# Kernel tuning notes

Measured on AMD Instinct MI355X. Metric: run time of the kernel, lower is better.

The kernel has to match this reference:

```python
import jax, jax.numpy as jnp
import numpy as np

B, S, H, DK, DV, DE = 2, 256, 8, 64, 64, 512
DT = H * DV
EPS = 1e-5

def _clin(xr, xi, W, b):
    # complex linear: x @ W + b with (re, im) parts; W: (2, d_in, d_out), b: (2, d_out)
    yr = xr @ W[0] - xi @ W[1] + b[0]
    yi = xr @ W[1] + xi @ W[0] + b[1]
    return yr, yi

def _emul(ar, ai, br, bi):
    # complex elementwise (Hadamard) multiply
    return ar * br - ai * bi, ar * bi + ai * br

def _forward(Z_q, Z_k, Z_v, t_measure_all, Wq, bq, Wk, bk, Wv, bv, Wp, bp,
             lambda_imag_v, lambda_real_v, lambda_omega_sqrt_v,
             lambda_gamma_sqrt_v, noise_floor, tau, eta_param):
    Bn = Z_q.shape[0]
    t = t_measure_all[0, :-1]
    t = t / (t[-1] - t[0])

    def heads(z, W, b, d):
        yr, yi = _clin(z[:, 0], z[:, 1], W, b)
        f = lambda a: a.reshape(Bn, S, H, d).swapaxes(-1, -2)  # (B,S,d,H)
        return f(yr), f(yi)

    Qr, Qi = heads(Z_q, Wq, bq, DK)
    Kr, Ki = heads(Z_k, Wk, bk, DK)
    Vr, Vi = heads(Z_v, Wv, bv, DV)

    # complex eigenvalues in conjugate pairs: (DV, H)
    lam_im = jnp.concatenate([lambda_imag_v, -lambda_imag_v], axis=1).T
    lam_re = jnp.broadcast_to(lambda_real_v[None, :], (DV, H))

    # forward/backward exponential kernels exp(+/- lambda t): (S, DV, H)
    phase = t[:, None, None] * lam_im[None]
    mag = jnp.exp(t[:, None, None] * lam_re[None])
    ef_r = mag * jnp.cos(phase); ef_i = mag * jnp.sin(phase)
    eb_r = jnp.cos(phase) / mag; eb_i = -jnp.sin(phase) / mag
    me_r, me_i = ef_r[0], ef_i[0]  # mat_exp

    # scalar covariance kernel per (i, j, head): process noise + measurement noise
    omega = lambda_omega_sqrt_v ** 2
    gamma = lambda_gamma_sqrt_v ** 2 + EPS
    dt = jnp.maximum(t[:, None] - t[None, :], 0.0)  # causal lags only
    den = 2.0 * lambda_real_v  # (H,)
    safe = jnp.where(jnp.abs(den) > 1e-6, den, 1.0)
    x = dt[:, :, None] * den
    g = jnp.where(jnp.abs(den) > 1e-6, jnp.expm1(x) / safe, dt[:, :, None])
    V_avg = omega * g + gamma * jnp.exp(x)  # (S,S,H)

    # factorized kernels: U_* = exp(-lambda t_j) * X_j ; propagator factor |exp(lambda t_i)|^2
    Uq_r, Uq_i = _emul(eb_r[None], eb_i[None], Qr, Qi)
    Uk_r, Uk_i = _emul(eb_r[None], eb_i[None], Kr, Ki)
    Uv_r, Uv_i = _emul(eb_r[None], eb_i[None], Vr, Vi)
    Vk2 = ef_r ** 2 + ef_i ** 2  # (S,DV,H)

    # precision-weighted residual norm |exp(lambda(t_i-t_j)) k_j - q_i|^2
    Uq2 = Uq_r ** 2 + Uq_i ** 2
    Uk2 = Uk_r ** 2 + Uk_i ** 2
    self_q = jnp.einsum('idh,bidh->bih', Vk2, Uq2)
    term_k = jnp.einsum('idh,bjdh->bijh', Vk2, Uk2)
    cross = (jnp.einsum('bidh,bjdh->bijh', Vk2[None] * Uq_r, Uk_r)
             + jnp.einsum('bidh,bjdh->bijh', Vk2[None] * Uq_i, Uk_i))
    R = term_k + self_q[:, :, None, :] - 2.0 * cross  # (B,S,S,H)

    base = (noise_floor ** 2 + EPS) * V_avg[None] + R
    scores = -(tau ** 2) * jnp.log(base)
    mask = jnp.tril(jnp.ones((S, S), bool))
    scores = jnp.where(mask[None, :, :, None], scores, -jnp.inf)
    attn = jax.nn.softmax(scores, axis=2)  # (B,S,S,H)

    # complex matmul with real-valued attention (imag part of Q_ij is zero)
    er = jnp.einsum('bijh,bjdh->bidh', attn, Uv_r)
    ei = jnp.einsum('bijh,bjdh->bidh', attn, Uv_i)
    est_r, est_i = _emul(ef_r[None], ef_i[None], er, ei)

    eta = jax.nn.sigmoid(eta_param)[0, 0]  # (1,DV,H)
    el_r = (1.0 - eta) * Vr + jax.nn.sigmoid(eta) * est_r
    el_i = (1.0 - eta) * Vi + jax.nn.sigmoid(eta) * est_i

    pr, pi = _emul(me_r[None, None], me_i[None, None], el_r, el_i)
    merge = lambda a: a.swapaxes(-1, -2).reshape(Bn, S, DT)
    o_r, o_i = _clin(merge(pr), merge(pi), Wp, bp)
    out = jnp.stack([o_r, o_i], axis=1)  # (B,2,S,DE)

    # all-pairs propagated estimates Z_ij = exp(lambda t_i) * U_v,j
    zr, zi = _emul(ef_r[None, :, None], ef_i[None, :, None],
                   Uv_r[:, None], Uv_i[:, None])  # (B,S,S,DV,H)
    zm = lambda a: a.swapaxes(-1, -2).reshape(Bn, S, S, DT)
    Z_ij = jnp.stack([zm(zr), zm(zi)], axis=1)  # (B,2,S,S,DT)

    est_latent = jnp.stack([el_r, el_i], axis=1)  # (B,2,S,DV,H)
    Q_ij = jnp.stack([attn, jnp.zeros_like(attn)], axis=1)
    epoch_lambdas = jnp.stack([lam_re, lam_im], 0).swapaxes(-1, -2).reshape(2, H * DV)[..., None]
    return est_latent, out, Q_ij, Z_ij, epoch_lambdas

def setup_inputs():
    key = jax.random.key(0)
    k = jax.random.split(key, 16)
    sc_in = 1.0 / np.sqrt(DE)
    sc_out = 1.0 / np.sqrt(DT)
    return {
        'Z_q': jax.random.normal(k[0], (B, 2, S, DE), jnp.float32),
        'Z_k': jax.random.normal(k[1], (B, 2, S, DE), jnp.float32),
        'Z_v': jax.random.normal(k[2], (B, 2, S, DE), jnp.float32),
        't_measure_all': jnp.arange(S + 1, dtype=jnp.float32)[None, :],
        'Wq': jax.random.normal(k[3], (2, DE, DT), jnp.float32) * sc_in,
        'bq': jax.random.normal(k[4], (2, DT), jnp.float32) * 0.01,
        'Wk': jax.random.normal(k[5], (2, DE, DT), jnp.float32) * sc_in,
        'bk': jax.random.normal(k[6], (2, DT), jnp.float32) * 0.01,
        'Wv': jax.random.normal(k[7], (2, DE, DT), jnp.float32) * sc_in,
        'bv': jax.random.normal(k[8], (2, DT), jnp.float32) * 0.01,
        'Wp': jax.random.normal(k[9], (2, DT, DE), jnp.float32) * sc_out,
        'bp': jax.random.normal(k[10], (2, DE), jnp.float32) * 0.01,
        'lambda_imag_v': jax.random.normal(k[11], (H, DV // 2), jnp.float32),
        'lambda_real_v': jax.random.normal(k[12], (H,), jnp.float32) * 0.5,
        'lambda_omega_sqrt_v': jax.random.normal(k[13], (H,), jnp.float32),
        'lambda_gamma_sqrt_v': jax.random.normal(k[14], (H,), jnp.float32),
        'noise_floor': jnp.ones((H,), jnp.float32),
        'tau': jnp.ones((H,), jnp.float32),
        'eta_param': jnp.zeros((1, 1, 1, DV, H), jnp.float32),
    }

def reference(Z_q, Z_k, Z_v, t_measure_all, Wq, bq, Wk, bk, Wv, bv, Wp, bp,
              lambda_imag_v, lambda_real_v, lambda_omega_sqrt_v,
              lambda_gamma_sqrt_v, noise_floor, tau, eta_param):
    return _forward(Z_q, Z_k, Z_v, t_measure_all, Wq, bq, Wk, bk, Wv, bv, Wp, bp,
                    lambda_imag_v, lambda_real_v, lambda_omega_sqrt_v,
                    lambda_gamma_sqrt_v, noise_floor, tau, eta_param)
```

## Files before the change

### kernel.cpp

```cpp
#include <hip/hip_runtime.h>
#include <hip/hip_bf16.h>
#include <math.h>

constexpr int kB  = 2;
constexpr int kS  = 256;
constexpr int kH  = 8;
constexpr float kEPS = 1e-5f;

constexpr int OFF_EST = 0;
constexpr int OFF_OUT = 524288;
constexpr int OFF_QIJ = 1048576;
constexpr int OFF_ZIJ = 3145728;
constexpr int OFF_EPO = 137363456;

constexpr int WS_EFR = 0;
constexpr int WS_EFI = 131072;
constexpr int WS_EBR = 262144;
constexpr int WS_EBI = 393216;
constexpr int WS_UQR = 524288;
constexpr int WS_UQI = 786432;
constexpr int WS_UKR = 1048576;
constexpr int WS_UKI = 1310720;
constexpr int WS_UVR = 1572864;
constexpr int WS_UVI = 1835008;
constexpr int WS_VR  = 2097152;
constexpr int WS_VI  = 2359296;
constexpr int WS_BF  = 3145728;

constexpr int A2Q = 0;
constexpr int A2K = 524288;
constexpr int A2V = 1048576;
constexpr int B2R0 = 1572864;

typedef __attribute__((ext_vector_type(8))) short bf16x8;
typedef __attribute__((ext_vector_type(4))) float f32x4;
typedef __attribute__((ext_vector_type(8))) unsigned short u16x8;
typedef __attribute__((ext_vector_type(4))) unsigned short u16x4;

__device__ __forceinline__ float sigm(float x) { return 1.f / (1.f + expf(-x)); }
__device__ __forceinline__ unsigned short f2b(float f) {
    __hip_bfloat16 h = __float2bfloat16(f);
    return *reinterpret_cast<unsigned short*>(&h);
}

__global__ __launch_bounds__(256) void k_precompute(
    const float* __restrict__ tall, const float* __restrict__ Lim,
    const float* __restrict__ Lre,
    float* __restrict__ efr, float* __restrict__ efi,
    float* __restrict__ ebr, float* __restrict__ ebi,
    float* __restrict__ epo)
{
    int idx = blockIdx.x * 256 + threadIdx.x;
    int s = idx >> 9;
    int c = idx & 511;
    int h = c >> 6;
    int d = c & 63;
    float li = (d < 32) ? Lim[h * 32 + d] : -Lim[h * 32 + d - 32];
    float lr = Lre[h];
    float t  = tall[s] / (tall[kS - 1] - tall[0]);
    float ph  = t * li;
    float mag = expf(t * lr);
    float cp  = cosf(ph);
    float sp  = sinf(ph);
    efr[idx] = mag * cp;
    efi[idx] = mag * sp;
    ebr[idx] = cp / mag;
    ebi[idx] = -sp / mag;
    if (s == 0) {
        epo[c]       = lr;
        epo[512 + c] = li;
    }
}

__global__ __launch_bounds__(256) void k_convA(
    const float* __restrict__ zq, const float* __restrict__ zk,
    const float* __restrict__ zv, __hip_bfloat16* __restrict__ bfbase)
{
    int idx = blockIdx.x * 256 + threadIdx.x;
    int tz  = idx >> 16;
    int rem = idx & 65535;
    int m   = rem >> 7;
    int k0  = (rem & 127) * 8;
    const float* src = (tz == 0) ? zq : (tz == 1) ? zk : zv;
    int b = m >> 8, s = m & 255;
    int c = (k0 >= 512) ? 1 : 0;
    int e = k0 - c * 512;
    const float* p = src + ((b * 2 + c) * 256 + s) * 512 + e;
    float4 v0 = *(const float4*)p;
    float4 v1 = *(const float4*)(p + 4);
    u16x8 o;
    o[0] = f2b(v0.x); o[1] = f2b(v0.y); o[2] = f2b(v0.z); o[3] = f2b(v0.w);
    o[4] = f2b(v1.x); o[5] = f2b(v1.y); o[6] = f2b(v1.z); o[7] = f2b(v1.w);
    __hip_bfloat16* dst = bfbase + ((tz == 0) ? A2Q : (tz == 1) ? A2K : A2V)
                          + m * 1024 + k0;
    *(u16x8*)dst = o;
}

__global__ __launch_bounds__(256) void k_convW(
    const float* __restrict__ wq, const float* __restrict__ wk,
    const float* __restrict__ wv, const float* __restrict__ wp,
    __hip_bfloat16* __restrict__ bfbase)
{
    __shared__ float s0[64][65];
    __shared__ float s1[64][65];
    const int z = blockIdx.z;
    const float* W  = (z == 0) ? wq : (z == 1) ? wk : (z == 2) ? wv : wp;
    const float* W0 = W;
    const float* W1 = W + 262144;
    const int k0 = blockIdx.x * 64;
    const int n0 = blockIdx.y * 64;
    const int kp = k0 & 511;
    const bool hf = (k0 >= 512);
    const int t = threadIdx.x;
    const int r = t >> 2;
    const int q = t & 3;
#pragma unroll
    for (int c = 0; c < 4; ++c) {
        int col = q * 16 + c * 4;
        *(float4*)&s0[r][col] = *(const float4*)&W0[(kp + r) * 512 + n0 + col];
        *(float4*)&s1[r][col] = *(const float4*)&W1[(kp + r) * 512 + n0 + col];
    }
    __syncthreads();
    u16x8 r0, r1, i0, i1;
#pragma unroll
    for (int u = 0; u < 8; ++u) {
        int kl = q * 16 + u;
        float w0 = s0[kl][r], w1 = s1[kl][r];
        r0[u] = f2b(hf ? -w1 : w0);
        i0[u] = f2b(hf ?  w0 : w1);
    }
#pragma unroll
    for (int u = 0; u < 8; ++u) {
        int kl = q * 16 + 8 + u;
        float w0 = s0[kl][r], w1 = s1[kl][r];
        r1[u] = f2b(hf ? -w1 : w0);
        i1[u] = f2b(hf ?  w0 : w1);
    }
    __hip_bfloat16* pr = bfbase + B2R0 + z * 1048576
                         + (size_t)(n0 + r) * 1024 + k0 + q * 16;
    __hip_bfloat16* pi = pr + 524288;
    *(u16x8*)pr       = r0;
    *(u16x8*)(pr + 8) = r1;
    *(u16x8*)pi       = i0;
    *(u16x8*)(pi + 8) = i1;
}

template<bool IS_P>
__global__ __launch_bounds__(256) void k_cmfma(
    const __hip_bfloat16* __restrict__ bfbase,
    const __hip_bfloat16* __restrict__ a2p,
    const float* __restrict__ bq, const float* __restrict__ bk,
    const float* __restrict__ bv, const float* __restrict__ bp,
    const float* __restrict__ ebr, const float* __restrict__ ebi,
    float* __restrict__ uqr, float* __restrict__ uqi,
    float* __restrict__ ukr, float* __restrict__ uki,
    float* __restrict__ uvr, float* __restrict__ uvi,
    float* __restrict__ vr,  float* __restrict__ vi,
    float* __restrict__ outp)
{
    __shared__ __align__(16) char sm[24576];
    char* sA  = sm;
    char* sBr = sm + 8192;
    char* sBi = sm + 16384;

    const int mode = IS_P ? 3 : (int)blockIdx.z;
    const __hip_bfloat16* A2 = IS_P ? a2p
        : bfbase + ((mode == 0) ? A2Q : (mode == 1) ? A2K : A2V);
    const __hip_bfloat16* Br = bfbase + B2R0 + mode * 1048576;
    const __hip_bfloat16* Bi = Br + 524288;
    const float* bias = IS_P ? bp : ((mode == 0) ? bq : (mode == 1) ? bk : bv);

    const int tid = threadIdx.x;
    const int m0 = blockIdx.y * 64;
    const int n0 = blockIdx.x * 64;
    const int lane = tid & 63;
    const int wv2 = tid >> 6;
    const int wr = wv2 >> 1, wc = wv2 & 1;
    const int lx = lane & 15, lhi = lane >> 4;

    const int srow  = tid >> 2;
    const int sslot = (tid & 3) * 32;

    const char* gA  = (const char*)(A2 + (size_t)(m0 + srow) * 1024);
    const char* gBr = (const char*)(Br + (size_t)(n0 + srow) * 1024);
    const char* gBi = (const char*)(Bi + (size_t)(n0 + srow) * 1024);
    const int swz = (srow & 7) << 4;
    char* dA  = sA  + srow * 128;
    char* dBr = sBr + srow * 128;
    char* dBi = sBi + srow * 128;

    f32x4 accR[2][2] = {};
    f32x4 accI[2][2] = {};

    int rowA[2], rowB[2];
    rowA[0] = wr * 32 + lx;  rowA[1] = rowA[0] + 16;
    rowB[0] = wc * 32 + lx;  rowB[1] = rowB[0] + 16;

    for (int kt = 0; kt < 16; ++kt) {
        const int kb = kt * 128;
        {
            float4 a0 = *(const float4*)(gA  + kb + sslot);
            float4 a1 = *(const float4*)(gA  + kb + sslot + 16);
            float4 b0 = *(const float4*)(gBr + kb + sslot);
            float4 b1 = *(const float4*)(gBr + kb + sslot + 16);
            float4 c0 = *(const float4*)(gBi + kb + sslot);
            float4 c1 = *(const float4*)(gBi + kb + sslot + 16);
            *(float4*)(dA  + ( sslot       ^ swz)) = a0;
            *(float4*)(dA  + ((sslot + 16) ^ swz)) = a1;
            *(float4*)(dBr + ( sslot       ^ swz)) = b0;
            *(float4*)(dBr + ((sslot + 16) ^ swz)) = b1;
            *(float4*)(dBi + ( sslot       ^ swz)) = c0;
            *(float4*)(dBi + ((sslot + 16) ^ swz)) = c1;
        }
        __syncthreads();
#pragma unroll
        for (int kk = 0; kk < 2; ++kk) {
            const int kbyte = kk * 64 + lhi * 16;
            bf16x8 af[2], brf[2], bif[2];
#pragma unroll
            for (int x = 0; x < 2; ++x) {
                int ra = rowA[x];
                af[x]  = *(const bf16x8*)(sA  + ra * 128 + (kbyte ^ ((ra & 7) << 4)));
                int rb = rowB[x];
                brf[x] = *(const bf16x8*)(sBr + rb * 128 + (kbyte ^ ((rb & 7) << 4)));
                bif[x] = *(const bf16x8*)(sBi + rb * 128 + (kbyte ^ ((rb & 7) << 4)));
            }
#pragma unroll
            for (int a = 0; a < 2; ++a)
#pragma unroll
                for (int bb = 0; bb < 2; ++bb) {
                    accR[a][bb] = __builtin_amdgcn_mfma_f32_16x16x32_bf16(
                        af[a], brf[bb], accR[a][bb], 0, 0, 0);
                    accI[a][bb] = __builtin_amdgcn_mfma_f32_16x16x32_bf16(
                        af[a], bif[bb], accI[a][bb], 0, 0, 0);
                }
        }
        __syncthreads();
    }

#pragma unroll
    for (int a = 0; a < 2; ++a) {
#pragma unroll
        for (int bb = 0; bb < 2; ++bb) {
#pragma unroll
            for (int j = 0; j < 4; ++j) {
                int m = m0 + wr * 32 + a * 16 + lhi * 4 + j;
                int n = n0 + wc * 32 + bb * 16 + lx;
                float yr = accR[a][bb][j] + bias[n];
                float yi = accI[a][bb][j] + bias[512 + n];
                int b = m >> 8, s = m & 255;
                if (IS_P) {
                    int rowo = m * 512 + b * 131072;
                    outp[rowo + n] = yr;
                    outp[rowo + 131072 + n] = yi;
                } else {
                    int h = n >> 6, d = n & 63;
                    float er_ = ebr[s * 512 + n], ei_ = ebi[s * 512 + n];
                    float ur = er_ * yr - ei_ * yi;
                    float ui = er_ * yi + ei_ * yr;
                    if (mode == 0) {
                        int idx = ((b * 8 + h) * 256 + s) * 64 + d;
                        uqr[idx] = ur; uqi[idx] = ui;
                    } else if (mode == 1) {
                        int idx = ((b * 8 + h) * 64 + d) * 256 + s;
                        ukr[idx] = ur; uki[idx] = ui;
                    } else {
                        int idx = ((b * 8 + h) * 256 + s) * 64 + d;
                        uvr[idx] = ur; uvi[idx] = ui;
                        int vidx = (b * 256 + s) * 512 + d * 8 + h;
                        vr[vidx] = yr; vi[vidx] = yi;
                    }
                }
            }
        }
    }
}

__global__ __launch_bounds__(256) void k_scores(
    const float* __restrict__ uqr, const float* __restrict__ uqi,
    const float* __restrict__ ukr, const float* __restrict__ uki,
    const float* __restrict__ tall,
    const float* __restrict__ Lre, const float* __restrict__ Lom,
    const float* __restrict__ Lga, const float* __restrict__ NF,
    const float* __restrict__ TAU,
    float* __restrict__ qij)
{
    __shared__ __align__(16) float sQr[32][68];
    __shared__ __align__(16) float sQi[32][68];
    __shared__ __align__(16) float sKr[64][32];
    __shared__ __align__(16) float sKi[64][32];

    int p = blockIdx.x;
    int it = 0;
    while (p > it) { p -= (it + 1); ++it; }
    const int jt = p;

    const int h = blockIdx.y, b = blockIdx.z;
    const int i0 = it * 32;
    const int j0 = jt * 32;
    const int tid = threadIdx.x;
    const int ti = tid >> 3;
    const int tj = tid & 7;

    {
        const float* src_r = uqr + ((b * 8 + h) * 256 + i0 + ti) * 64;
        const float* src_i = uqi + ((b * 8 + h) * 256 + i0 + ti) * 64;
        *(float4*)&sQr[ti][tj * 4]      = *(const float4*)&src_r[tj * 4];
        *(float4*)&sQr[ti][32 + tj * 4] = *(const float4*)&src_r[32 + tj * 4];
        *(float4*)&sQi[ti][tj * 4]      = *(const float4*)&src_i[tj * 4];
        *(float4*)&sQi[ti][32 + tj * 4] = *(const float4*)&src_i[32 + tj * 4];
    }
    {
        const int kr2 = tid >> 2;
        const int kq2 = tid & 3;
        const float* ksrc_r = ukr + ((b * 8 + h) * 64 + kr2) * 256 + j0;
        const float* ksrc_i = uki + ((b * 8 + h) * 64 + kr2) * 256 + j0;
        *(float4*)&sKr[kr2][kq2 * 4]      = *(const float4*)&ksrc_r[kq2 * 4];
        *(float4*)&sKr[kr2][16 + kq2 * 4] = *(const float4*)&ksrc_r[16 + kq2 * 4];
        *(float4*)&sKi[kr2][kq2 * 4]      = *(const float4*)&ksrc_i[kq2 * 4];
        *(float4*)&sKi[kr2][16 + kq2 * 4] = *(const float4*)&ksrc_i[16 + kq2 * 4];
    }

    const float lre  = Lre[h];
    const float om   = Lom[h] * Lom[h];
    const float ga   = Lga[h] * Lga[h] + kEPS;
    const float nf2  = NF[h] * NF[h] + kEPS;
    const float tau2 = TAU[h] * TAU[h];
    const float den  = 2.f * lre;
    const float invT = 1.f / (tall[kS - 1] - tall[0]);
    const int   i    = i0 + ti;
    const float t_i  = tall[i] * invT;
    const float m2i  = expf(2.f * t_i * lre);
    const bool  denok = fabsf(den) > 1e-6f;

    __syncthreads();

    float acc[4] = {0.f, 0.f, 0.f, 0.f};
#pragma unroll 16
    for (int d = 0; d < 64; d++) {
        float qr = sQr[ti][d];
        float qi = sQi[ti][d];
        float4 kr = *(float4*)&sKr[d][tj * 4];
        float4 ki = *(float4*)&sKi[d][tj * 4];
#define DSTEP(c, KRC, KIC)                                    \
        { float dr = qr - KRC; float di = qi - KIC;           \
          acc[c] = fmaf(dr, dr, acc[c]);                      \
          acc[c] = fmaf(di, di, acc[c]); }
        DSTEP(0, kr.x, ki.x)
        DSTEP(1, kr.y, ki.y)
        DSTEP(2, kr.z, ki.z)
        DSTEP(3, kr.w, ki.w)
#undef DSTEP
    }

#pragma unroll
    for (int c = 0; c < 4; c++) {
        int j = j0 + tj * 4 + c;
        if (j <= i) {
            float t_j = tall[j] * invT;
            float dtt = fmaxf(t_i - t_j, 0.f);
            float x = dtt * den;
            float g = denok ? (expm1f(x) / den) : dtt;
            float Vv = om * g + ga * expf(x);
            float base = nf2 * Vv + m2i * acc[c];
            qij[((b * 512 + i) * 256 + j) * 8 + h] = -tau2 * logf(base);
        }
    }
}

__global__ __launch_bounds__(256) void k_zij_smpv(
    const float* __restrict__ efr, const float* __restrict__ efi,
    const float* __restrict__ uvr, const float* __restrict__ uvi,
    float* __restrict__ zout,
    float* __restrict__ qij,
    const float* __restrict__ vr,  const float* __restrict__ vi,
    const float* __restrict__ ETA,
    float* __restrict__ out_est, __hip_bfloat16* __restrict__ a2p)
{
    __shared__ float sP[32][257];
    __shared__ __align__(16) float sVr[32][64];
    __shared__ __align__(16) float sVi[32][64];

    const int bid = blockIdx.x;
    const int tid = threadIdx.x;

    if (bid >= 128) {
        const int z  = bid - 128;
        const int j0 = (z & 63) * 4;
        const int i  = (z >> 6) & 255;
        const int b  = z >> 14;
#pragma unroll
        for (int half = 0; half < 2; half++) {
            int dt = half * 256 + tid;
            float fr = efr[i * 512 + dt];
            float fi = efi[i * 512 + dt];
            int h = dt >> 6, d = dt & 63;
            const float* ur = uvr + ((b * 8 + h) * 256) * 64 + d;
            const float* ui = uvi + ((b * 8 + h) * 256) * 64 + d;
#pragma unroll
            for (int jj = 0; jj < 4; jj++) {
                int j = j0 + jj;
                float vr_ = ur[j * 64];
                float vi_ = ui[j * 64];
                float zr = fr * vr_ - fi * vi_;
                float zi = fr * vi_ + fi * vr_;
                int idx0 = (b * 2) * 33554432 + i * 131072 + j * 512 + dt;
                __builtin_nontemporal_store(zr, &zout[idx0]);
                __builtin_nontemporal_store(zi, &zout[idx0 + 33554432]);
            }
        }
        return;
    }

    const int it = bid & 7;
    const int h  = (bid >> 3) & 7;
    const int b  = bid >> 6;
    const int i0 = it * 32;
    const int ti = tid >> 3;
    const int tj = tid & 7;
    const int i  = i0 + ti;

    float* srow = qij + ((b * 512 + i) * 256) * 8 + h;
    float mx = -1e30f;
    for (int j = tj; j <= i; j += 8) {
        float v = srow[j * 8];
        sP[ti][j] = v;
        mx = fmaxf(mx, v);
    }
#pragma unroll
    for (int m = 1; m < 8; m <<= 1) mx = fmaxf(mx, __shfl_xor(mx, m));
    float sum = 0.f;
    for (int j = tj; j <= i; j += 8) {
        float e = expf(sP[ti][j] - mx);
        sP[ti][j] = e;
        sum += e;
    }
#pragma unroll
    for (int m = 1; m < 8; m <<= 1) sum += __shfl_xor(sum, m);
    const float inv = 1.f / sum;

    float* qi_out = qij + ((b * 512 + 256 + i) * 256) * 8 + h;
    const int jfill = i0 + 32;
    for (int j = tj; j < 256; j += 8) {
        float p = 0.f;
        if (j <= i) p = sP[ti][j] * inv;
        if (j < jfill) sP[ti][j] = p;
        srow[j * 8]   = p;
        qi_out[j * 8] = 0.f;
    }
    __syncthreads();

    const int dl = tid & 7;
    float accR[8] = {0.f}, accI[8] = {0.f};

    for (int jt = 0; jt <= it; jt++) {
        const int j0 = jt * 32;
        {
            const float* sr = uvr + ((b * 8 + h) * 256 + j0 + ti) * 64;
            const float* si = uvi + ((b * 8 + h) * 256 + j0 + ti) * 64;
            *(float4*)&sVr[ti][dl * 4]      = *(const float4*)&sr[dl * 4];
            *(float4*)&sVr[ti][32 + dl * 4] = *(const float4*)&sr[32 + dl * 4];
            *(float4*)&sVi[ti][dl * 4]      = *(const float4*)&si[dl * 4];
            *(float4*)&sVi[ti][32 + dl * 4] = *(const float4*)&si[32 + dl * 4];
        }
        __syncthreads();

#pragma unroll 8
        for (int jj = 0; jj < 32; jj++) {
            float a = sP[ti][j0 + jj];
            float4 v0 = *(float4*)&sVr[jj][dl * 8];
            float4 v1 = *(float4*)&sVr[jj][dl * 8 + 4];
            float4 w0 = *(float4*)&sVi[jj][dl * 8];
            float4 w1 = *(float4*)&sVi[jj][dl * 8 + 4];
            float vv[8] = {v0.x, v0.y, v0.z, v0.w, v1.x, v1.y, v1.z, v1.w};
            float ww[8] = {w0.x, w0.y, w0.z, w0.w, w1.x, w1.y, w1.z, w1.w};
#pragma unroll
            for (int c = 0; c < 8; c++) {
                accR[c] = fmaf(a, vv[c], accR[c]);
                accI[c] = fmaf(a, ww[c], accI[c]);
            }
        }
        __syncthreads();
    }

    const int cb = h * 64 + dl * 8;
    f32x4 fr0 = *(const f32x4*)&efr[i * 512 + cb];
    f32x4 fr1 = *(const f32x4*)&efr[i * 512 + cb + 4];
    f32x4 fi0 = *(const f32x4*)&efi[i * 512 + cb];
    f32x4 fi1 = *(const f32x4*)&efi[i * 512 + cb + 4];
    f32x4 mr0 = *(const f32x4*)&efr[cb];
    f32x4 mr1 = *(const f32x4*)&efr[cb + 4];
    f32x4 mi0 = *(const f32x4*)&efi[cb];
    f32x4 mi1 = *(const f32x4*)&efi[cb + 4];

    u16x8 o_r, o_i;
#pragma unroll
    for (int c = 0; c < 8; c++) {
        float fr = (c < 4) ? fr0[c] : fr1[c - 4];
        float fi = (c < 4) ? fi0[c] : fi1[c - 4];
        float mr = (c < 4) ? mr0[c] : mr1[c - 4];
        float mi = (c < 4) ? mi0[c] : mi1[c - 4];
        int p = dl * 64 + c * 8 + h;
        float estr = fr * accR[c] - fi * accI[c];
        float esti = fr * accI[c] + fi * accR[c];
        float et = sigm(ETA[p]);
        float w1 = 1.f - et;
        float w2 = sigm(et);
        float vr_ = vr[(b * 256 + i) * 512 + p];
        float vi_ = vi[(b * 256 + i) * 512 + p];
        float elr = w1 * vr_ + w2 * estr;
        float eli = w1 * vi_ + w2 * esti;
        out_est[((b * 2 + 0) * 256 + i) * 512 + p] = elr;
        out_est[((b * 2 + 1) * 256 + i) * 512 + p] = eli;
        o_r[c] = f2b(mr * elr - mi * eli);
        o_i[c] = f2b(mr * eli + mi * elr);
    }
    __hip_bfloat16* ap = a2p + (b * 256 + i) * 1024 + cb;
    *(u16x8*)ap         = o_r;
    *(u16x8*)(ap + 512) = o_i;
}

extern "C" void kernel_launch(void* const* d_in, const int* in_sizes, int n_in,
                              void* d_out, int out_size, void* d_ws, size_t ws_size,
                              hipStream_t stream)
{
    const float* Zq   = (const float*)d_in[0];
    const float* Zk   = (const float*)d_in[1];
    const float* Zv   = (const float*)d_in[2];
    const float* tall = (const float*)d_in[3];
    const float* Wq   = (const float*)d_in[4];
    const float* bq   = (const float*)d_in[5];
    const float* Wk   = (const float*)d_in[6];
    const float* bk   = (const float*)d_in[7];
    const float* Wv   = (const float*)d_in[8];
    const float* bv   = (const float*)d_in[9];
    const float* Wp   = (const float*)d_in[10];
    const float* bp   = (const float*)d_in[11];
    const float* Lim  = (const float*)d_in[12];
    const float* Lre  = (const float*)d_in[13];
    const float* Lom  = (const float*)d_in[14];
    const float* Lga  = (const float*)d_in[15];
    const float* NF   = (const float*)d_in[16];
    const float* TAU  = (const float*)d_in[17];
    const float* ETA  = (const float*)d_in[18];

    float* out = (float*)d_out;
    float* ws  = (float*)d_ws;

    float* efr = ws + WS_EFR; float* efi = ws + WS_EFI;
    float* ebr = ws + WS_EBR; float* ebi = ws + WS_EBI;
    float* uqr = ws + WS_UQR; float* uqi = ws + WS_UQI;
    float* ukr = ws + WS_UKR; float* uki = ws + WS_UKI;
    float* uvr = ws + WS_UVR; float* uvi = ws + WS_UVI;
    float* vr  = ws + WS_VR;  float* vi  = ws + WS_VI;
    __hip_bfloat16* bfbase = (__hip_bfloat16*)(ws + WS_BF);
    __hip_bfloat16* a2p    = (__hip_bfloat16*)(ws + WS_EBR);

    k_precompute<<<512, 256, 0, stream>>>(tall, Lim, Lre, efr, efi, ebr, ebi,
                                          out + OFF_EPO);
    k_convA<<<768, 256, 0, stream>>>(Zq, Zk, Zv, bfbase);
    k_convW<<<dim3(16, 8, 4), 256, 0, stream>>>(Wq, Wk, Wv, Wp, bfbase);

    k_cmfma<false><<<dim3(8, 8, 3), 256, 0, stream>>>(
        bfbase, nullptr, bq, bk, bv, bp, ebr, ebi,
        uqr, uqi, ukr, uki, uvr, uvi, vr, vi, nullptr);

    k_scores<<<dim3(36, 8, 2), 256, 0, stream>>>(uqr, uqi, ukr, uki, tall,
                                                 Lre, Lom, Lga, NF, TAU,
                                                 out + OFF_QIJ);

    k_zij_smpv<<<32896, 256, 0, stream>>>(
        efr, efi, uvr, uvi, out + OFF_ZIJ,
        out + OFF_QIJ, vr, vi, ETA, out + OFF_EST, a2p);

    k_cmfma<true><<<dim3(8, 8, 1), 256, 0, stream>>>(
        bfbase, a2p, bq, bk, bv, bp, ebr, ebi,
        nullptr, nullptr, nullptr, nullptr, nullptr, nullptr, nullptr, nullptr,
        out + OFF_OUT);
}
```

Measured before the change: 153.6 us.

## Fuse score computation into softmax/PV attention blocks, keeping scores in shared memory

The separate k_scores kernel is removed and its distance-based score computation is moved into the attention blocks of the combined zij/softmax kernel. Each attention block loops over key tiles up to its causal limit, computes log-kernel scores directly into shared memory, and skips the global write-then-read of scores before softmax. This drops a launch and a global round trip, but it serializes score tiles within each of the 128 attention blocks, reducing parallelism, and it enlarges shared memory (aliasing K and V buffers) to about 66KB, which may reduce occupancy.

Result: faster. 145.4 us (-5.4%).

```diff
diff --git a/kernel.cpp b/kernel.cpp
--- a/kernel.cpp
+++ b/kernel.cpp
@@ -276,110 +276,29 @@
     }
 }
 
-__global__ __launch_bounds__(256) void k_scores(
+__global__ __launch_bounds__(256) void k_zij_attn(
+    const float* __restrict__ efr, const float* __restrict__ efi,
+    const float* __restrict__ uvr, const float* __restrict__ uvi,
+    float* __restrict__ zout,
     const float* __restrict__ uqr, const float* __restrict__ uqi,
     const float* __restrict__ ukr, const float* __restrict__ uki,
     const float* __restrict__ tall,
     const float* __restrict__ Lre, const float* __restrict__ Lom,
     const float* __restrict__ Lga, const float* __restrict__ NF,
     const float* __restrict__ TAU,
-    float* __restrict__ qij)
-{
-    __shared__ __align__(16) float sQr[32][68];
-    __shared__ __align__(16) float sQi[32][68];
-    __shared__ __align__(16) float sKr[64][32];
-    __shared__ __align__(16) float sKi[64][32];
-
-    int p = blockIdx.x;
-    int it = 0;
-    while (p > it) { p -= (it + 1); ++it; }
-    const int jt = p;
-
-    const int h = blockIdx.y, b = blockIdx.z;
-    const int i0 = it * 32;
-    const int j0 = jt * 32;
-    const int tid = threadIdx.x;
-    const int ti = tid >> 3;
-    const int tj = tid & 7;
-
-    {
-        const float* src_r = uqr + ((b * 8 + h) * 256 + i0 + ti) * 64;
-        const float* src_i = uqi + ((b * 8 + h) * 256 + i0 + ti) * 64;
-        *(float4*)&sQr[ti][tj * 4]      = *(const float4*)&src_r[tj * 4];
-        *(float4*)&sQr[ti][32 + tj * 4] = *(const float4*)&src_r[32 + tj * 4];
-        *(float4*)&sQi[ti][tj * 4]      = *(const float4*)&src_i[tj * 4];
-        *(float4*)&sQi[ti][32 + tj * 4] = *(const float4*)&src_i[32 + tj * 4];
-    }
-    {
-        const int kr2 = tid >> 2;
-        const int kq2 = tid & 3;
-        const float* ksrc_r = ukr + ((b * 8 + h) * 64 + kr2) * 256 + j0;
-        const float* ksrc_i = uki + ((b * 8 + h) * 64 + kr2) * 256 + j0;
-        *(float4*)&sKr[kr2][kq2 * 4]      = *(const float4*)&ksrc_r[kq2 * 4];
-        *(float4*)&sKr[kr2][16 + kq2 * 4] = *(const float4*)&ksrc_r[16 + kq2 * 4];
-        *(float4*)&sKi[kr2][kq2 * 4]      = *(const float4*)&ksrc_i[kq2 * 4];
-        *(float4*)&sKi[kr2][16 + kq2 * 4] = *(const float4*)&ksrc_i[16 + kq2 * 4];
-    }
-
-    const float lre  = Lre[h];
-    const float om   = Lom[h] * Lom[h];
-    const float ga   = Lga[h] * Lga[h] + kEPS;
-    const float nf2  = NF[h] * NF[h] + kEPS;
-    const float tau2 = TAU[h] * TAU[h];
-    const float den  = 2.f * lre;
-    const float invT = 1.f / (tall[kS - 1] - tall[0]);
-    const int   i    = i0 + ti;
-    const float t_i  = tall[i] * invT;
-    const float m2i  = expf(2.f * t_i * lre);
-    const bool  denok = fabsf(den) > 1e-6f;
-
-    __syncthreads();
-
-    float acc[4] = {0.f, 0.f, 0.f, 0.f};
-#pragma unroll 16
-    for (int d = 0; d < 64; d++) {
-        float qr = sQr[ti][d];
-        float qi = sQi[ti][d];
-        float4 kr = *(float4*)&sKr[d][tj * 4];
-        float4 ki = *(float4*)&sKi[d][tj * 4];
-#define DSTEP(c, KRC, KIC)                                    \
-        { float dr = qr - KRC; float di = qi - KIC;           \
-          acc[c] = fmaf(dr, dr, acc[c]);                      \
-          acc[c] = fmaf(di, di, acc[c]); }
-        DSTEP(0, kr.x, ki.x)
-        DSTEP(1, kr.y, ki.y)
-        DSTEP(2, kr.z, ki.z)
-        DSTEP(3, kr.w, ki.w)
-#undef DSTEP
-    }
-
-#pragma unroll
-    for (int c = 0; c < 4; c++) {
-        int j = j0 + tj * 4 + c;
-        if (j <= i) {
-            float t_j = tall[j] * invT;
-            float dtt = fmaxf(t_i - t_j, 0.f);
-            float x = dtt * den;
-            float g = denok ? (expm1f(x) / den) : dtt;
-            float Vv = om * g + ga * expf(x);
-            float base = nf2 * Vv + m2i * acc[c];
-            qij[((b * 512 + i) * 256 + j) * 8 + h] = -tau2 * logf(base);
-        }
-    }
-}
-
-__global__ __launch_bounds__(256) void k_zij_smpv(
-    const float* __restrict__ efr, const float* __restrict__ efi,
-    const float* __restrict__ uvr, const float* __restrict__ uvi,
-    float* __restrict__ zout,
     float* __restrict__ qij,
     const float* __restrict__ vr,  const float* __restrict__ vi,
     const float* __restrict__ ETA,
     float* __restrict__ out_est, __hip_bfloat16* __restrict__ a2p)
 {
-    __shared__ float sP[32][257];
-    __shared__ __align__(16) float sVr[32][64];
-    __shared__ __align__(16) float sVi[32][64];
+    __shared__ __align__(16) char smem[66688];
+    float (*sP)[257] = (float(*)[257])smem;
+    float (*sKr)[32] = (float(*)[32])(smem + 32896);
+    float (*sKi)[32] = (float(*)[32])(smem + 41088);
+    float (*sQr)[68] = (float(*)[68])(smem + 49280);
+    float (*sQi)[68] = (float(*)[68])(smem + 57984);
+    float (*sVr)[64] = (float(*)[64])(smem + 32896);
+    float (*sVi)[64] = (float(*)[64])(smem + 41088);
 
     const int bid = blockIdx.x;
     const int tid = threadIdx.x;
@@ -420,13 +339,78 @@
     const int tj = tid & 7;
     const int i  = i0 + ti;
 
-    float* srow = qij + ((b * 512 + i) * 256) * 8 + h;
+    {
+        const float* qsr = uqr + ((b * 8 + h) * 256 + i) * 64;
+        const float* qsi = uqi + ((b * 8 + h) * 256 + i) * 64;
+        *(float4*)&sQr[ti][tj * 4]      = *(const float4*)&qsr[tj * 4];
+        *(float4*)&sQr[ti][32 + tj * 4] = *(const float4*)&qsr[32 + tj * 4];
+        *(float4*)&sQi[ti][tj * 4]      = *(const float4*)&qsi[tj * 4];
+        *(float4*)&sQi[ti][32 + tj * 4] = *(const float4*)&qsi[32 + tj * 4];
+    }
+
+    const float lre  = Lre[h];
+    const float om   = Lom[h] * Lom[h];
+    const float ga   = Lga[h] * Lga[h] + kEPS;
+    const float nf2  = NF[h] * NF[h] + kEPS;
+    const float tau2 = TAU[h] * TAU[h];
+    const float den  = 2.f * lre;
+    const float invT = 1.f / (tall[kS - 1] - tall[0]);
+    const float t_i  = tall[i] * invT;
+    const float m2i  = expf(2.f * t_i * lre);
+    const bool  denok = fabsf(den) > 1e-6f;
+
+    const int kr2 = tid >> 2;
+    const int kq2 = tid & 3;
+
+    for (int jt = 0; jt <= it; ++jt) {
+        const int j0 = jt * 32;
+        __syncthreads();
+        {
+            const float* ksrc_r = ukr + ((b * 8 + h) * 64 + kr2) * 256 + j0;
+            const float* ksrc_i = uki + ((b * 8 + h) * 64 + kr2) * 256 + j0;
+            *(float4*)&sKr[kr2][kq2 * 4]      = *(const float4*)&ksrc_r[kq2 * 4];
+            *(float4*)&sKr[kr2][16 + kq2 * 4] = *(const float4*)&ksrc_r[16 + kq2 * 4];
+            *(float4*)&sKi[kr2][kq2 * 4]      = *(const float4*)&ksrc_i[kq2 * 4];
+            *(float4*)&sKi[kr2][16 + kq2 * 4] = *(const float4*)&ksrc_i[16 + kq2 * 4];
+        }
+        __syncthreads();
+
+        float acc[4] = {0.f, 0.f, 0.f, 0.f};
+#pragma unroll 16
+        for (int d = 0; d < 64; d++) {
+            float qr = sQr[ti][d];
+            float qi = sQi[ti][d];
+            float4 kr = *(float4*)&sKr[d][tj * 4];
+            float4 ki = *(float4*)&sKi[d][tj * 4];
+#define DSTEP(c, KRC, KIC)                                    \
+            { float dr = qr - KRC; float di = qi - KIC;       \
+              acc[c] = fmaf(dr, dr, acc[c]);                  \
+              acc[c] = fmaf(di, di, acc[c]); }
+            DSTEP(0, kr.x, ki.x)
+            DSTEP(1, kr.y, ki.y)
+            DSTEP(2, kr.z, ki.z)
+            DSTEP(3, kr.w, ki.w)
+#undef DSTEP
+        }
+
+#pragma unroll
+        for (int c = 0; c < 4; c++) {
+            int j = j0 + tj * 4 + c;
+            if (j <= i) {
+                float t_j = tall[j] * invT;
+                float dtt = fmaxf(t_i - t_j, 0.f);
+                float x = dtt * den;
+                float g = denok ? (expm1f(x) / den) : dtt;
+                float Vv = om * g + ga * expf(x);
+                float base = nf2 * Vv + m2i * acc[c];
+                sP[ti][j] = -tau2 * logf(base);
+            }
+        }
+    }
+    __syncthreads();
+
     float mx = -1e30f;
-    for (int j = tj; j <= i; j += 8) {
-        float v = srow[j * 8];
-        sP[ti][j] = v;
-        mx = fmaxf(mx, v);
-    }
+    for (int j = tj; j <= i; j += 8) mx = fmaxf(mx, sP[ti][j]);
 #pragma unroll
     for (int m = 1; m < 8; m <<= 1) mx = fmaxf(mx, __shfl_xor(mx, m));
     float sum = 0.f;
@@ -439,6 +423,7 @@
     for (int m = 1; m < 8; m <<= 1) sum += __shfl_xor(sum, m);
     const float inv = 1.f / sum;
 
+    float* srow   = qij + ((b * 512 + i) * 256) * 8 + h;
     float* qi_out = qij + ((b * 512 + 256 + i) * 256) * 8 + h;
     const int jfill = i0 + 32;
     for (int j = tj; j < 256; j += 8) {
@@ -565,12 +550,9 @@
         bfbase, nullptr, bq, bk, bv, bp, ebr, ebi,
         uqr, uqi, ukr, uki, uvr, uvi, vr, vi, nullptr);
 
-    k_scores<<<dim3(36, 8, 2), 256, 0, stream>>>(uqr, uqi, ukr, uki, tall,
-                                                 Lre, Lom, Lga, NF, TAU,
-                                                 out + OFF_QIJ);
-
-    k_zij_smpv<<<32896, 256, 0, stream>>>(
+    k_zij_attn<<<32896, 256, 0, stream>>>(
         efr, efi, uvr, uvi, out + OFF_ZIJ,
+        uqr, uqi, ukr, uki, tall, Lre, Lom, Lga, NF, TAU,
         out + OFF_QIJ, vr, vi, ETA, out + OFF_EST, a2p);
 
     k_cmfma<true><<<dim3(8, 8, 1), 256, 0, stream>>>(
```
